# Performance work log

Measured on AMD Instinct MI355X. Metric: run time of the kernel, lower is better.

Reference implementation:

```python
import jax, jax.numpy as jnp
import numpy as np
from jax import lax

B, T, D, H, O = 32, 512, 512, 1024, 512


def setup_inputs() -> dict:
    key = jax.random.key(0)
    ks = jax.random.split(key, 7)
    s = lambda fan_in: 1.0 / np.sqrt(fan_in)
    return {
        "x": jax.random.normal(ks[0], (B, T, D), jnp.float32),
        "Wx0": jax.random.normal(ks[1], (D, 4 * H), jnp.float32) * s(D),
        "Wh0": jax.random.normal(ks[2], (H, 4 * H), jnp.float32) * s(H),
        "b0": jnp.zeros((4 * H,), jnp.float32),
        "Wx1": jax.random.normal(ks[3], (H, 4 * H), jnp.float32) * s(H),
        "Wh1": jax.random.normal(ks[4], (H, 4 * H), jnp.float32) * s(H),
        "b1": jnp.zeros((4 * H,), jnp.float32),
        "Wd": jax.random.normal(ks[5], (H, O), jnp.float32) * s(H),
        "bd": jnp.zeros((O,), jnp.float32),
    }


def _lstm_cell(c, h, inp, Wx, Wh, b):
    # flax OptimizedLSTMCell: fused gate GEMM, gate order i, f, g, o
    z = inp @ Wx + h @ Wh + b  # [B, 4H]
    i, f, g, o = jnp.split(z, 4, axis=-1)
    c_new = jax.nn.sigmoid(f) * c + jax.nn.sigmoid(i) * jnp.tanh(g)
    h_new = jax.nn.sigmoid(o) * jnp.tanh(c_new)
    return c_new, h_new


def reference(x, Wx0, Wh0, b0, Wx1, Wh1, b1, Wd, bd):
    b = x.shape[0]
    h = Wh0.shape[0]
    zero = jnp.zeros((b, h), x.dtype)
    carry0 = ((zero, zero), (zero, zero))  # ((c0, h0), (c1, h1)), zeros like flax default

    def step(carry, xt):
        (c0, h0), (c1, h1) = carry
        c0, h0 = _lstm_cell(c0, h0, xt, Wx0, Wh0, b0)
        c1, h1 = _lstm_cell(c1, h1, h0, Wx1, Wh1, b1)
        return ((c0, h0), (c1, h1)), h1

    xs = jnp.swapaxes(x, 0, 1)  # [T, B, D] for scan over time
    _, ys = lax.scan(step, carry0, xs)
    y = jnp.swapaxes(ys, 0, 1)  # [B, T, H]
    return y @ Wd + bd  # [B, T, O]
```

## Files before the change

kernel.cpp:

```cpp
#include <hip/hip_runtime.h>


typedef _Float16 half8  __attribute__((ext_vector_type(8)));
typedef float    floatx4 __attribute__((ext_vector_type(4)));

#define WREC_OFF   0UL
#define WX0_OFF    25165824UL
#define WD_OFF     29360128UL
#define XH_OFF     30408704UL
#define H1_OFF     47185920UL
#define H0_OFF     80740352UL
#define FLAGS_OFF  114294784UL

__device__ __forceinline__ float fsig(float x){ return 1.0f/(1.0f + __expf(-x)); }
__device__ __forceinline__ float ftanhf(float x){
  float e = __expf(2.0f*fabsf(x));
  float r = 1.0f - 2.0f/(e + 1.0f);
  return copysignf(r, x);
}

__global__ void conv_wrec(const float* __restrict__ Wh0,
                          const float* __restrict__ Wx1,
                          const float* __restrict__ Wh1,
                          _Float16* __restrict__ out){
  int idx = blockIdx.x*256 + threadIdx.x;
  if (idx >= 256*3*128*16) return;
  int c  = idx & 15;
  int t1 = idx >> 4;
  int kc = t1 & 127;
  int t2 = t1 >> 7;
  int mat = t2 % 3;
  int wg  = t2 / 3;
  const float* W = (mat==0) ? Wh0 : (mat==1) ? Wx1 : Wh1;
  int col = (c>>2)*1024 + wg*4 + (c&3);
  _Float16* o = out + (size_t)idx*8;
  #pragma unroll
  for (int j=0;j<8;++j) o[j] = (_Float16)W[(kc*8+j)*4096 + col];
}

__global__ void conv_wx0(const float* __restrict__ W, _Float16* __restrict__ out){
  int idx = blockIdx.x*256 + threadIdx.x;
  if (idx >= 256*64*16) return;
  int c  = idx & 15;
  int kc = (idx >> 4) & 63;
  int wg = idx >> 10;
  int col = (c>>2)*1024 + wg*4 + (c&3);
  _Float16* o = out + (size_t)idx*8;
  #pragma unroll
  for (int j=0;j<8;++j) o[j] = (_Float16)W[(kc*8+j)*4096 + col];
}

__global__ void conv_wd(const float* __restrict__ W, _Float16* __restrict__ out){
  int idx = blockIdx.x*256 + threadIdx.x;
  if (idx >= 32*128*16) return;
  int c  = idx & 15;
  int kc = (idx >> 4) & 127;
  int nt = idx >> 11;
  int col = nt*16 + c;
  _Float16* o = out + (size_t)idx*8;
  #pragma unroll
  for (int j=0;j<8;++j) o[j] = (_Float16)W[(kc*8+j)*512 + col];
}

__global__ void conv_x(const float* __restrict__ x, _Float16* __restrict__ xh){
  int idx = blockIdx.x*256 + threadIdx.x;
  if (idx >= 2097152) return;
  int dq = idx & 127;
  int bt = idx >> 7;
  int b  = bt & 31;
  int t  = bt >> 5;
  float4 v = ((const float4*)x)[(size_t)(b*512 + t)*128 + dq];
  _Float16* o = xh + (size_t)idx*4;
  o[0]=(_Float16)v.x; o[1]=(_Float16)v.y; o[2]=(_Float16)v.z; o[3]=(_Float16)v.w;
}

#define AF(base, ks)  (*(const half8*)((base) + (ks)*32))
#define BF(w, ks)     (*(const half8*)((w) + (((ks)*4 + q)*16 + c)*8))

__device__ __forceinline__ void gates_store(floatx4 acc, float* cs,
    _Float16* dst, int g, int c, int mt, int q, int wg){
  #pragma unroll
  for (int r=0;r<4;++r){
    float v0 = acc[r];
    float v1 = __shfl_xor(v0, 4, 64);
    float v2 = __shfl_xor(v0, 8, 64);
    float v3 = __shfl_xor(v1, 8, 64);
    float zi = (g==0)?v0:(g==1)?v1:(g==2)?v2:v3;
    float zf = (g==0)?v1:(g==1)?v0:(g==2)?v3:v2;
    float zg = (g==0)?v2:(g==1)?v3:(g==2)?v0:v1;
    float zo = (g==0)?v3:(g==1)?v2:(g==2)?v1:v0;
    float cn = fsig(zf)*cs[r] + fsig(zi)*ftanhf(zg);
    cs[r] = cn;
    float hv = fsig(zo)*ftanhf(cn);
    unsigned hb16 = (unsigned)__builtin_bit_cast(unsigned short, (_Float16)hv);
    unsigned up   = (unsigned)__shfl_xor((int)hb16, 1, 64);
    if (g==0 && (c&1)==0)
      __hip_atomic_store((unsigned*)(dst + (mt*16 + q*4 + r)*1024 + wg*4 + c),
                         hb16 | (up<<16),
                         __ATOMIC_RELAXED, __HIP_MEMORY_SCOPE_AGENT);
  }
}

__global__ __launch_bounds__(128, 1) void lstm_persist(
    const _Float16* __restrict__ wrec, const _Float16* __restrict__ wx0a,
    const _Float16* __restrict__ xh,
    const float* __restrict__ b0g, const float* __restrict__ b1g,
    _Float16* __restrict__ h0a, _Float16* __restrict__ h1a,
    unsigned int* __restrict__ flags)
{
  extern __shared__ _Float16 lds[];
  _Float16* w0  = lds;
  _Float16* w1  = lds + 16384;
  _Float16* w2  = lds + 32768;
  _Float16* w3  = lds + 49152;

  const int wg = blockIdx.x, tid = threadIdx.x;
  const int wv = tid>>6, l = tid&63, q = l>>4, c = l&15;
  const int g = (c>>2);
  const int mt = wv;
  const int row = mt*16 + c;
  const int grp = wg >> 3;

  unsigned int* gcnt = flags + grp*64;
  unsigned int* root = flags + 2048;
  unsigned int* go   = flags + 4096;

  {
    const uint4* srcA = (const uint4*)(wrec + (size_t)wg*49152);
    const uint4* srcB = (const uint4*)(wx0a + (size_t)wg*8192);
    uint4* dst = (uint4*)lds;
    for (int i=tid; i<6144; i+=128) dst[i] = srcA[i];
    for (int i=tid; i<1024; i+=128) dst[6144+i] = srcB[i];
  }
  float c0[4] = {0,0,0,0}, c1[4] = {0,0,0,0};
  const float b0v = b0g[g*1024 + wg*4 + (c&3)];
  const float b1v = b1g[g*1024 + wg*4 + (c&3)];
  __syncthreads();

  {
    const _Float16* xb = xh + (size_t)row*512 + q*8;
    floatx4 p0={b0v,b0v,b0v,b0v}, p1={0,0,0,0};
    #pragma unroll
    for (int s=0; s<8; ++s){
      p0 = __builtin_amdgcn_mfma_f32_16x16x32_f16(AF(xb,s),   BF(w3,s),   p0,0,0,0);
      p1 = __builtin_amdgcn_mfma_f32_16x16x32_f16(AF(xb,8+s), BF(w3,8+s), p1,0,0,0);
    }
    floatx4 z = p0+p1;
    gates_store(z, c0, h0a, g, c, mt, q, wg);
  }

  for (int t=0; t<512; ++t){
    __syncthreads();

    const unsigned tgt = (unsigned)(t+1);
    if (tid==0){
      unsigned o = __hip_atomic_fetch_add(gcnt, 1u, __ATOMIC_RELAXED,
                                          __HIP_MEMORY_SCOPE_AGENT);
      if (o == 8u*tgt - 1u){
        unsigned r = __hip_atomic_fetch_add(root, 1u, __ATOMIC_RELAXED,
                                            __HIP_MEMORY_SCOPE_AGENT);
        if (r == 32u*tgt - 1u){
          #pragma unroll
          for (int g2=0; g2<32; ++g2)
            __hip_atomic_store(go + g2*64, tgt, __ATOMIC_RELAXED,
                               __HIP_MEMORY_SCOPE_AGENT);
        }
      }
    }

    int tn = (t<511) ? t+1 : 511;
    const _Float16* xb = xh + (size_t)(tn*32 + row)*512 + q*8;
    half8 X[16];
    #pragma unroll
    for (int s=0; s<16; ++s) X[s] = AF(xb, s);
    floatx4 aA0={b0v,b0v,b0v,b0v}, aA1={0,0,0,0};
    #pragma unroll
    for (int s=0; s<8; ++s){
      aA0 = __builtin_amdgcn_mfma_f32_16x16x32_f16(X[s],   BF(w3,s),   aA0,0,0,0);
      aA1 = __builtin_amdgcn_mfma_f32_16x16x32_f16(X[8+s], BF(w3,8+s), aA1,0,0,0);
    }

    if (tid==0){
      while (__hip_atomic_load(go + grp*64, __ATOMIC_RELAXED,
                               __HIP_MEMORY_SCOPE_AGENT) < tgt)
        __builtin_amdgcn_s_sleep(1);
    }
    __syncthreads();

    const _Float16* h0c = h0a + (size_t)t*32768 + row*1024 + q*8;
    const _Float16* h1p = h1a + (size_t)(t-1)*32768 + row*1024 + q*8;
    half8 H1[32], H0[32];
    if (t > 0){
      #pragma unroll
      for (int s=0; s<32; ++s) H1[s] = AF(h1p, s);
    }
    #pragma unroll
    for (int s=0; s<32; ++s) H0[s] = AF(h0c, s);

    floatx4 aB0={b1v,b1v,b1v,b1v}, aB1={0,0,0,0};
    floatx4 aC0={0,0,0,0}, aC1={0,0,0,0};
    if (t > 0){
      #pragma unroll
      for (int s=0; s<16; ++s){
        aC0 = __builtin_amdgcn_mfma_f32_16x16x32_f16(H1[s],    BF(w2,s),    aC0,0,0,0);
        aC1 = __builtin_amdgcn_mfma_f32_16x16x32_f16(H1[16+s], BF(w2,16+s), aC1,0,0,0);
      }
    }
    #pragma unroll
    for (int s=0; s<16; ++s){
      aB0 = __builtin_amdgcn_mfma_f32_16x16x32_f16(H0[s],    BF(w1,s),    aB0,0,0,0);
      aB1 = __builtin_amdgcn_mfma_f32_16x16x32_f16(H0[16+s], BF(w1,16+s), aB1,0,0,0);
      aA0 = __builtin_amdgcn_mfma_f32_16x16x32_f16(H0[s],    BF(w0,s),    aA0,0,0,0);
      aA1 = __builtin_amdgcn_mfma_f32_16x16x32_f16(H0[16+s], BF(w0,16+s), aA1,0,0,0);
    }
    {
      floatx4 z1 = (aB0+aB1)+(aC0+aC1);
      gates_store(z1, c1, h1a + (size_t)t*32768, g, c, mt, q, wg);
    }
    if (t < 511){
      floatx4 z0 = aA0+aA1;
      gates_store(z0, c0, h0a + (size_t)(t+1)*32768, g, c, mt, q, wg);
    }
  }
}

__global__ __launch_bounds__(256) void wd_gemm(const _Float16* __restrict__ h1a,
                                               const _Float16* __restrict__ wda,
                                               const float* __restrict__ bd,
                                               float* __restrict__ y){
  int mb = blockIdx.x;
  int nb = blockIdx.y;
  int tid = threadIdx.x, wv = tid>>6, l = tid&63, q = l>>4, c = l&15;
  int mt = wv & 1, nh = wv >> 1;
  floatx4 acc[4];
  #pragma unroll
  for (int gg=0; gg<4; ++gg) acc[gg] = (floatx4){0.f,0.f,0.f,0.f};
  const _Float16* arow = h1a + (size_t)(mb*32 + mt*16 + c)*1024;
  #pragma unroll 4
  for (int ks=0; ks<32; ++ks){
    int kc = ks*4 + q;
    half8 a = *(const half8*)(arow + kc*8);
    #pragma unroll
    for (int gg=0; gg<4; ++gg){
      int nt = nb*8 + nh*4 + gg;
      half8 b = *(const half8*)(wda + ((size_t)(nt*128 + kc)*16 + c)*8);
      acc[gg] = __builtin_amdgcn_mfma_f32_16x16x32_f16(a,b,acc[gg],0,0,0);
    }
  }
  #pragma unroll
  for (int gg=0; gg<4; ++gg){
    int o = nb*128 + nh*64 + gg*16 + c;
    float bdv = bd[o];
    #pragma unroll
    for (int r=0;r<4;++r){
      int row = mb*32 + mt*16 + q*4 + r;
      int tt = row >> 5, bb = row & 31;
      y[(size_t)bb*262144 + tt*512 + o] = acc[gg][r] + bdv;
    }
  }
}

extern "C" void kernel_launch(void* const* d_in, const int* in_sizes, int n_in,
                              void* d_out, int out_size, void* d_ws, size_t ws_size,
                              hipStream_t stream){
  const float* x   = (const float*)d_in[0];
  const float* Wx0 = (const float*)d_in[1];
  const float* Wh0 = (const float*)d_in[2];
  const float* b0  = (const float*)d_in[3];
  const float* Wx1 = (const float*)d_in[4];
  const float* Wh1 = (const float*)d_in[5];
  const float* b1  = (const float*)d_in[6];
  const float* Wd  = (const float*)d_in[7];
  const float* bd  = (const float*)d_in[8];
  float* y = (float*)d_out;
  char* ws = (char*)d_ws;

  _Float16* wrec = (_Float16*)(ws + WREC_OFF);
  _Float16* wx0a = (_Float16*)(ws + WX0_OFF);
  _Float16* wda  = (_Float16*)(ws + WD_OFF);
  _Float16* xh   = (_Float16*)(ws + XH_OFF);
  _Float16* h1a  = (_Float16*)(ws + H1_OFF);
  _Float16* h0a  = (_Float16*)(ws + H0_OFF);
  unsigned int* flags = (unsigned int*)(ws + FLAGS_OFF);

  hipMemsetAsync(flags, 0, 24576, stream);
  conv_wrec<<<dim3(6144), dim3(256), 0, stream>>>(Wh0, Wx1, Wh1, wrec);
  conv_wx0 <<<dim3(1024), dim3(256), 0, stream>>>(Wx0, wx0a);
  conv_wd  <<<dim3(256),  dim3(256), 0, stream>>>(Wd, wda);
  conv_x   <<<dim3(8192), dim3(256), 0, stream>>>(x, xh);
  hipFuncSetAttribute((const void*)lstm_persist,
                      hipFuncAttributeMaxDynamicSharedMemorySize, 114688);
  lstm_persist<<<dim3(256), dim3(128), 114688, stream>>>(wrec, wx0a, xh, b0, b1,
                                                         h0a, h1a, flags);
  wd_gemm  <<<dim3(512,4), dim3(256), 0, stream>>>(h1a, wda, bd, y);
}
```

Baseline: 5.167 ms.

## Split grid barrier into separate layer-0 and layer-1 barriers to shorten critical path

Replaces the single per-step grid barrier with two independent hierarchical barriers, one for layer-0 hidden states and one for layer-1. Layer 0 for the next step is computed and published right after h0 is available, before the layer-1 work. Layer 1 waits only on the previous layer-1 barrier. This is meant to shorten the serial dependency chain per timestep by letting layer-0 of step t+1 overlap layer-1 of step t. In exchange there are two barriers per step instead of one, more __syncthreads calls, and a larger flag region to zero.

After: 5.731 ms. 1.11x slower.

```diff
diff --git a/kernel.cpp b/kernel.cpp
--- a/kernel.cpp
+++ b/kernel.cpp
@@ -76,6 +76,24 @@
 
 #define AF(base, ks)  (*(const half8*)((base) + (ks)*32))
 #define BF(w, ks)     (*(const half8*)((w) + (((ks)*4 + q)*16 + c)*8))
+
+#define ARRIVE(gcnt, root, go, tgt)                                          \
+  { unsigned o_ = __hip_atomic_fetch_add((gcnt), 1u, __ATOMIC_RELAXED,       \
+                                         __HIP_MEMORY_SCOPE_AGENT);          \
+    if (o_ == 8u*(tgt) - 1u){                                                \
+      unsigned r_ = __hip_atomic_fetch_add((root), 1u, __ATOMIC_RELAXED,     \
+                                           __HIP_MEMORY_SCOPE_AGENT);        \
+      if (r_ == 32u*(tgt) - 1u){                                             \
+        _Pragma("unroll")                                                    \
+        for (int g2=0; g2<32; ++g2)                                          \
+          __hip_atomic_store((go) + g2*64, (tgt), __ATOMIC_RELAXED,          \
+                             __HIP_MEMORY_SCOPE_AGENT);                      \
+      } } }
+
+#define POLL(p, tgt)                                                         \
+  while (__hip_atomic_load((p), __ATOMIC_RELAXED,                            \
+                           __HIP_MEMORY_SCOPE_AGENT) < (tgt))                \
+    __builtin_amdgcn_s_sleep(1);
 
 __device__ __forceinline__ void gates_store(floatx4 acc, float* cs,
     _Float16* dst, int g, int c, int mt, int q, int wg){
@@ -121,9 +139,12 @@
   const int row = mt*16 + c;
   const int grp = wg >> 3;
 
-  unsigned int* gcnt = flags + grp*64;
-  unsigned int* root = flags + 2048;
-  unsigned int* go   = flags + 4096;
+  unsigned int* gcntA = flags + grp*64;
+  unsigned int* rootA = flags + 2048;
+  unsigned int* goA   = flags + 4096;
+  unsigned int* gcntB = flags + 8192 + grp*64;
+  unsigned int* rootB = flags + 8192 + 2048;
+  unsigned int* goB   = flags + 8192 + 4096;
 
   {
     const uint4* srcA = (const uint4*)(wrec + (size_t)wg*49152);
@@ -148,78 +169,86 @@
     floatx4 z = p0+p1;
     gates_store(z, c0, h0a, g, c, mt, q, wg);
   }
+  __syncthreads();
+  if (tid==0) ARRIVE(gcntA, rootA, goA, 1u);
+
+  floatx4 xA0, xA1;
+  {
+    const _Float16* xb = xh + (size_t)(32 + row)*512 + q*8;
+    half8 X[16];
+    #pragma unroll
+    for (int s=0; s<16; ++s) X[s] = AF(xb, s);
+    xA0=(floatx4){b0v,b0v,b0v,b0v}; xA1=(floatx4){0,0,0,0};
+    #pragma unroll
+    for (int s=0; s<8; ++s){
+      xA0 = __builtin_amdgcn_mfma_f32_16x16x32_f16(X[s],   BF(w3,s),   xA0,0,0,0);
+      xA1 = __builtin_amdgcn_mfma_f32_16x16x32_f16(X[8+s], BF(w3,8+s), xA1,0,0,0);
+    }
+  }
 
   for (int t=0; t<512; ++t){
+    const unsigned tA = (unsigned)(t+1);
+
+    if (tid==0){ POLL(goA + grp*64, tA); }
     __syncthreads();
 
-    const unsigned tgt = (unsigned)(t+1);
-    if (tid==0){
-      unsigned o = __hip_atomic_fetch_add(gcnt, 1u, __ATOMIC_RELAXED,
-                                          __HIP_MEMORY_SCOPE_AGENT);
-      if (o == 8u*tgt - 1u){
-        unsigned r = __hip_atomic_fetch_add(root, 1u, __ATOMIC_RELAXED,
-                                            __HIP_MEMORY_SCOPE_AGENT);
-        if (r == 32u*tgt - 1u){
-          #pragma unroll
-          for (int g2=0; g2<32; ++g2)
-            __hip_atomic_store(go + g2*64, tgt, __ATOMIC_RELAXED,
-                               __HIP_MEMORY_SCOPE_AGENT);
-        }
+    const _Float16* h0c = h0a + (size_t)t*32768 + row*1024 + q*8;
+    half8 H0[32];
+    #pragma unroll
+    for (int s=0; s<32; ++s) H0[s] = AF(h0c, s);
+
+    if (t < 511){
+      floatx4 aA0=xA0, aA1=xA1;
+      #pragma unroll
+      for (int s=0; s<16; ++s){
+        aA0 = __builtin_amdgcn_mfma_f32_16x16x32_f16(H0[s],    BF(w0,s),    aA0,0,0,0);
+        aA1 = __builtin_amdgcn_mfma_f32_16x16x32_f16(H0[16+s], BF(w0,16+s), aA1,0,0,0);
       }
-    }
-
-    int tn = (t<511) ? t+1 : 511;
-    const _Float16* xb = xh + (size_t)(tn*32 + row)*512 + q*8;
-    half8 X[16];
-    #pragma unroll
-    for (int s=0; s<16; ++s) X[s] = AF(xb, s);
-    floatx4 aA0={b0v,b0v,b0v,b0v}, aA1={0,0,0,0};
-    #pragma unroll
-    for (int s=0; s<8; ++s){
-      aA0 = __builtin_amdgcn_mfma_f32_16x16x32_f16(X[s],   BF(w3,s),   aA0,0,0,0);
-      aA1 = __builtin_amdgcn_mfma_f32_16x16x32_f16(X[8+s], BF(w3,8+s), aA1,0,0,0);
-    }
-
-    if (tid==0){
-      while (__hip_atomic_load(go + grp*64, __ATOMIC_RELAXED,
-                               __HIP_MEMORY_SCOPE_AGENT) < tgt)
-        __builtin_amdgcn_s_sleep(1);
-    }
-    __syncthreads();
-
-    const _Float16* h0c = h0a + (size_t)t*32768 + row*1024 + q*8;
-    const _Float16* h1p = h1a + (size_t)(t-1)*32768 + row*1024 + q*8;
-    half8 H1[32], H0[32];
-    if (t > 0){
-      #pragma unroll
-      for (int s=0; s<32; ++s) H1[s] = AF(h1p, s);
-    }
-    #pragma unroll
-    for (int s=0; s<32; ++s) H0[s] = AF(h0c, s);
-
-    floatx4 aB0={b1v,b1v,b1v,b1v}, aB1={0,0,0,0};
+      floatx4 z0 = aA0+aA1;
+      gates_store(z0, c0, h0a + (size_t)(t+1)*32768, g, c, mt, q, wg);
+      __syncthreads();
+      if (tid==0) ARRIVE(gcntA, rootA, goA, tA+1);
+    }
+
     floatx4 aC0={0,0,0,0}, aC1={0,0,0,0};
     if (t > 0){
+      if (tid==0){ POLL(goB + grp*64, (unsigned)t); }
+      __syncthreads();
+      const _Float16* h1p = h1a + (size_t)(t-1)*32768 + row*1024 + q*8;
+      half8 H1[32];
+      #pragma unroll
+      for (int s=0; s<32; ++s) H1[s] = AF(h1p, s);
       #pragma unroll
       for (int s=0; s<16; ++s){
         aC0 = __builtin_amdgcn_mfma_f32_16x16x32_f16(H1[s],    BF(w2,s),    aC0,0,0,0);
         aC1 = __builtin_amdgcn_mfma_f32_16x16x32_f16(H1[16+s], BF(w2,16+s), aC1,0,0,0);
       }
     }
+    floatx4 aB0={b1v,b1v,b1v,b1v}, aB1={0,0,0,0};
     #pragma unroll
     for (int s=0; s<16; ++s){
       aB0 = __builtin_amdgcn_mfma_f32_16x16x32_f16(H0[s],    BF(w1,s),    aB0,0,0,0);
       aB1 = __builtin_amdgcn_mfma_f32_16x16x32_f16(H0[16+s], BF(w1,16+s), aB1,0,0,0);
-      aA0 = __builtin_amdgcn_mfma_f32_16x16x32_f16(H0[s],    BF(w0,s),    aA0,0,0,0);
-      aA1 = __builtin_amdgcn_mfma_f32_16x16x32_f16(H0[16+s], BF(w0,16+s), aA1,0,0,0);
     }
     {
       floatx4 z1 = (aB0+aB1)+(aC0+aC1);
       gates_store(z1, c1, h1a + (size_t)t*32768, g, c, mt, q, wg);
     }
+    __syncthreads();
+    if (tid==0) ARRIVE(gcntB, rootB, goB, tA);
+
     if (t < 511){
-      floatx4 z0 = aA0+aA1;
-      gates_store(z0, c0, h0a + (size_t)(t+1)*32768, g, c, mt, q, wg);
+      int tn = (t+2 < 512) ? t+2 : 511;
+      const _Float16* xb = xh + (size_t)(tn*32 + row)*512 + q*8;
+      half8 X[16];
+      #pragma unroll
+      for (int s=0; s<16; ++s) X[s] = AF(xb, s);
+      xA0=(floatx4){b0v,b0v,b0v,b0v}; xA1=(floatx4){0,0,0,0};
+      #pragma unroll
+      for (int s=0; s<8; ++s){
+        xA0 = __builtin_amdgcn_mfma_f32_16x16x32_f16(X[s],   BF(w3,s),   xA0,0,0,0);
+        xA1 = __builtin_amdgcn_mfma_f32_16x16x32_f16(X[8+s], BF(w3,8+s), xA1,0,0,0);
+      }
     }
   }
 }
@@ -283,7 +312,7 @@
   _Float16* h0a  = (_Float16*)(ws + H0_OFF);
   unsigned int* flags = (unsigned int*)(ws + FLAGS_OFF);
 
-  hipMemsetAsync(flags, 0, 24576, stream);
+  hipMemsetAsync(flags, 0, 65536, stream);
   conv_wrec<<<dim3(6144), dim3(256), 0, stream>>>(Wh0, Wx1, Wh1, wrec);
   conv_wx0 <<<dim3(1024), dim3(256), 0, stream>>>(Wx0, wx0a);
   conv_wd  <<<dim3(256),  dim3(256), 0, stream>>>(Wd, wda);
```
